# Performance work log

Hardware: AMD Instinct MI355X
Metric: run time of the kernel (lower is better)

## Reference

```python
import jax, jax.numpy as jnp
import numpy as np

L = 28          # layers
D = 1024        # hidden
HQ = 16         # query heads
HKV = 8         # kv heads
HD = 128        # head dim
DFF = 3072      # mlp intermediate
Q = 512         # prefill length (= end_step, past_kv_len = 0)
EPS = 1e-6


def setup_inputs() -> dict:
    key = jax.random.key(0)
    ks = jax.random.split(key, 12)
    s = 0.02
    hidden_states = jax.random.normal(ks[0], (1, Q, D), jnp.float32)
    # RoPE tables (concatenated-halves layout, base 1e6 as in Qwen3)
    pos = jnp.arange(Q, dtype=jnp.float32)
    inv_freq = 1.0 / (1e6 ** (jnp.arange(0, HD, 2, dtype=jnp.float32) / HD))
    freqs = pos[:, None] * inv_freq[None, :]              # [Q, HD/2]
    emb = jnp.concatenate([freqs, freqs], axis=-1)        # [Q, HD]
    position_cos = jnp.cos(emb)[None]                     # [1, Q, HD]
    position_sin = jnp.sin(emb)[None]
    # causal mask: 0 where key_pos <= query_pos else -1e9 ; [1,1,Q,Q]
    i = jnp.arange(Q)
    attention_mask = jnp.where(i[None, :] <= i[:, None], 0.0, -1e9).astype(jnp.float32)[None, None]
    # stacked per-layer weights (torch Linear y = x @ W^T stored here as [in,out])
    Wq = jax.random.normal(ks[1], (L, D, HQ * HD), jnp.float32) * s
    Wk = jax.random.normal(ks[2], (L, D, HKV * HD), jnp.float32) * s
    Wv = jax.random.normal(ks[3], (L, D, HKV * HD), jnp.float32) * s
    Wo = jax.random.normal(ks[4], (L, HQ * HD, D), jnp.float32) * s
    Wg = jax.random.normal(ks[5], (L, D, DFF), jnp.float32) * s
    Wu = jax.random.normal(ks[6], (L, D, DFF), jnp.float32) * s
    Wd = jax.random.normal(ks[7], (L, DFF, D), jnp.float32) * s
    ln1 = jnp.ones((L, D), jnp.float32)
    ln2 = jnp.ones((L, D), jnp.float32)
    qn = jnp.ones((L, HD), jnp.float32)
    kn = jnp.ones((L, HD), jnp.float32)
    return {"hidden_states": hidden_states, "position_cos": position_cos,
            "position_sin": position_sin, "attention_mask": attention_mask,
            "Wq": Wq, "Wk": Wk, "Wv": Wv, "Wo": Wo, "Wg": Wg, "Wu": Wu, "Wd": Wd,
            "ln1": ln1, "ln2": ln2, "qn": qn, "kn": kn}


def rmsnorm(x, w):
    return x * jax.lax.rsqrt(jnp.mean(x * x, axis=-1, keepdims=True) + EPS) * w


def rotate_half(x):
    x1, x2 = jnp.split(x, 2, axis=-1)
    return jnp.concatenate([-x2, x1], axis=-1)


def reference(hidden_states, position_cos, position_sin, attention_mask,
              Wq, Wk, Wv, Wo, Wg, Wu, Wd, ln1, ln2, qn, kn):
    q_len = hidden_states.shape[1]
    scale = 1.0 / np.sqrt(HD)
    cos = position_cos[:, None]   # [1,1,Q,HD] broadcast over heads
    sin = position_sin[:, None]

    def layer(h, p):
        wq, wk, wv, wo, wg, wu, wd, l1, l2, qw, kw = p
        x = rmsnorm(h, l1)
        q = (x @ wq).reshape(1, q_len, HQ, HD).transpose(0, 2, 1, 3)   # [1,HQ,Q,HD]
        k = (x @ wk).reshape(1, q_len, HKV, HD).transpose(0, 2, 1, 3)  # [1,HKV,Q,HD]
        v = (x @ wv).reshape(1, q_len, HKV, HD).transpose(0, 2, 1, 3)
        q = rmsnorm(q, qw)
        k = rmsnorm(k, kw)
        q = q * cos + rotate_half(q) * sin
        k = k * cos + rotate_half(k) * sin
        # fp16 KV-cache round trip (faithful to k.half() store / .float() load)
        k = k.astype(jnp.float16).astype(jnp.float32)
        v = v.astype(jnp.float16).astype(jnp.float32)
        # GQA: repeat kv heads
        k = jnp.repeat(k, HQ // HKV, axis=1)
        v = jnp.repeat(v, HQ // HKV, axis=1)
        scores = jnp.einsum('bhqd,bhkd->bhqk', q, k) * scale + attention_mask
        probs = jax.nn.softmax(scores, axis=-1)
        attn = jnp.einsum('bhqk,bhkd->bhqd', probs, v)
        attn = attn.transpose(0, 2, 1, 3).reshape(1, q_len, HQ * HD)
        h = h + attn @ wo
        y = rmsnorm(h, l2)
        h = h + (jax.nn.silu(y @ wg) * (y @ wu)) @ wd
        return h, None

    params = (Wq, Wk, Wv, Wo, Wg, Wu, Wd, ln1, ln2, qn, kn)
    out, _ = jax.lax.scan(layer, hidden_states, params)
    return out
```

## Files before the change

### kernel.cpp

```cpp
#include <hip/hip_runtime.h>
#include <stdint.h>


typedef __bf16 bf16_t;
typedef _Float16 f16_t;
typedef __bf16 bf16x8 __attribute__((ext_vector_type(8)));
typedef __bf16 bf16x4 __attribute__((ext_vector_type(4)));
typedef _Float16 f16x8 __attribute__((ext_vector_type(8)));
typedef _Float16 f16x4 __attribute__((ext_vector_type(4)));
typedef float f32x4 __attribute__((ext_vector_type(4)));

#define SEQ 512
#define NHQ 16
#define NHKV 8
#define HD 128

#define IMG_QKV 0ull
#define IMG_WO  8388608ull
#define IMG_GU  12582912ull
#define IMG_WD  25165824ull
#define IMG_LAYER_BYTES 31457280ull

typedef const __attribute__((address_space(1))) uint32_t as1_u32;
typedef __attribute__((address_space(3))) uint32_t as3_u32;

__device__ __forceinline__ void gload16(const void* g, void* l) {
    __builtin_amdgcn_global_load_lds((as1_u32*)g, (as3_u32*)l, 16, 0, 0);
}

__device__ __forceinline__ size_t aoff(int row, int col, int ldak) {
    return (((size_t)((row >> 6) * ldak + (col >> 6))) << 13) +
           ((size_t)(row & 63) << 7) +
           (size_t)((((col & 63) << 1)) ^ ((row & 7) << 4));
}

__global__ __launch_bounds__(256) void k_copy(const float* __restrict__ src,
                                              float* __restrict__ dst)
{
    size_t i = ((size_t)blockIdx.x * 256 + threadIdx.x) * 4;
    *(float4*)(dst + i) = *(const float4*)(src + i);
}

__device__ __forceinline__ void conv_tile(
    int b, int lay,
    const float* __restrict__ Wq, const float* __restrict__ Wk,
    const float* __restrict__ Wv, const float* __restrict__ Wo,
    const float* __restrict__ Wg, const float* __restrict__ Wu,
    const float* __restrict__ Wd, char* __restrict__ ib, void* smemv)
{
    const float* wq = Wq + (size_t)lay * 1024 * 2048;
    const float* wk = Wk + (size_t)lay * 1024 * 1024;
    const float* wv = Wv + (size_t)lay * 1024 * 1024;
    const float* wo = Wo + (size_t)lay * 2048 * 1024;
    const float* wg = Wg + (size_t)lay * 1024 * 3072;
    const float* wu = Wu + (size_t)lay * 1024 * 3072;
    const float* wd = Wd + (size_t)lay * 3072 * 1024;

    const float* src = nullptr;
    int ldbw = 0, n, kt, guMode = 0;
    size_t dstoff;
    if (b < 1024) {
        n = b >> 4; kt = b & 15;
        int C0 = n * 64;
        if (C0 < 2048)      { src = wq + C0;          ldbw = 2048; }
        else if (C0 < 3072) { src = wk + (C0 - 2048); ldbw = 1024; }
        else                { src = wv + (C0 - 3072); ldbw = 1024; }
        src += (size_t)(kt * 64) * ldbw;
        dstoff = IMG_QKV + (size_t)b * 8192;
    } else if (b < 1536) {
        int b2 = b - 1024; n = b2 >> 5; kt = b2 & 31;
        src = wo + (size_t)(kt * 64) * 1024 + n * 64; ldbw = 1024;
        dstoff = IMG_WO + (size_t)b2 * 8192;
    } else if (b < 3072) {
        int b3 = b - 1536; n = b3 >> 4; kt = b3 & 15;
        guMode = 1; ldbw = 3072;
        dstoff = IMG_GU + (size_t)b3 * 8192;
    } else {
        int b4 = b - 3072; n = b4 / 48; kt = b4 % 48;
        src = wd + (size_t)(kt * 64) * 1024 + n * 64; ldbw = 1024;
        dstoff = IMG_WD + (size_t)b4 * 8192;
    }

    float (*T)[68] = (float (*)[68])smemv;
    int tid = threadIdx.x;
    if (!guMode) {
#pragma unroll
        for (int it = 0; it < 4; ++it) {
            int idx = it * 256 + tid;
            int kk = idx >> 4, seg = idx & 15;
            *(float4*)&T[kk][seg * 4] = *(const float4*)(src + (size_t)kk * ldbw + seg * 4);
        }
    } else {
        const float* wg_ = wg + (size_t)(kt * 64) * 3072;
        const float* wu_ = wu + (size_t)(kt * 64) * 3072;
#pragma unroll
        for (int it = 0; it < 4; ++it) {
            int idx = it * 256 + tid;
            int kk = idx >> 4, seg = idx & 15;
            int nl = seg * 4;
            int colc = n * 32 + ((nl >> 5) & 1) * 16 + (nl & 15);
            const float* s2 = (((nl >> 4) & 1) ? wu_ : wg_) + (size_t)kk * 3072 + colc;
            *(float4*)&T[kk][nl] = *(const float4*)s2;
        }
    }
    __syncthreads();
    char* dst = ib + dstoff;
#pragma unroll
    for (int it = 0; it < 2; ++it) {
        int kg = tid & 7;
        int nrow = it * 32 + (tid >> 3);
        bf16x8 o;
#pragma unroll
        for (int j = 0; j < 8; ++j) o[j] = (bf16_t)T[kg * 8 + j][nrow];
        *(bf16x8*)(dst + nrow * 128 + ((kg * 16) ^ ((nrow & 7) << 4))) = o;
    }
}

__global__ __launch_bounds__(256) void k_conv(
    int lay,
    const float* __restrict__ Wq, const float* __restrict__ Wk,
    const float* __restrict__ Wv, const float* __restrict__ Wo,
    const float* __restrict__ Wg, const float* __restrict__ Wu,
    const float* __restrict__ Wd, char* __restrict__ img)
{
    __shared__ __align__(16) char smem[17408];
    conv_tile(blockIdx.x, lay, Wq, Wk, Wv, Wo, Wg, Wu, Wd, img, smem);
}

__global__ __launch_bounds__(256) void k_rms(
    float* __restrict__ h, const bf16_t* __restrict__ parts, int nparts,
    const float* __restrict__ w, char* __restrict__ ximg)
{
    int t = blockIdx.x, tid = threadIdx.x;
    size_t base = (size_t)t * 1024 + tid * 4;
    float4 v = *(const float4*)(h + base);
    for (int p = 0; p < nparts; ++p) {
        bf16x4 a = *(const bf16x4*)(parts + (size_t)p * 524288 + base);
        v.x += (float)a[0]; v.y += (float)a[1]; v.z += (float)a[2]; v.w += (float)a[3];
    }
    if (nparts) *(float4*)(h + base) = v;
    float ss = v.x * v.x + v.y * v.y + v.z * v.z + v.w * v.w;
#pragma unroll
    for (int m = 1; m < 64; m <<= 1) ss += __shfl_xor(ss, m);
    __shared__ float red[4];
    if ((tid & 63) == 0) red[tid >> 6] = ss;
    __syncthreads();
    float tot = (red[0] + red[1]) + (red[2] + red[3]);
    float sc = rsqrtf(tot * (1.0f / 1024.0f) + 1e-6f);
    float4 wv4 = *(const float4*)(w + tid * 4);
    bf16x4 o;
    o[0] = (bf16_t)(v.x * sc * wv4.x);
    o[1] = (bf16_t)(v.y * sc * wv4.y);
    o[2] = (bf16_t)(v.z * sc * wv4.z);
    o[3] = (bf16_t)(v.w * sc * wv4.w);
    *(bf16x4*)(ximg + aoff(t, tid * 4, 16)) = o;
}

__global__ __launch_bounds__(256) void k_finalize(
    const float* __restrict__ h, const bf16_t* __restrict__ parts,
    float* __restrict__ out)
{
    size_t base = ((size_t)blockIdx.x * 256 + threadIdx.x) * 4;
    float4 v = *(const float4*)(h + base);
#pragma unroll
    for (int p = 0; p < 4; ++p) {
        bf16x4 a = *(const bf16x4*)(parts + (size_t)p * 524288 + base);
        v.x += (float)a[0]; v.y += (float)a[1]; v.z += (float)a[2]; v.w += (float)a[3];
    }
    *(float4*)(out + base) = v;
}

template <int NBN, int SPLITK, int MODE, int LDAK>
__device__ __forceinline__ void gemm_core(
    const char* __restrict__ Aimg, const char* __restrict__ Bimg,
    void* __restrict__ outp, char* smem, int f)
{
    const int steps = LDAK / SPLITK;
    int bm = f / (NBN * SPLITK);
    int r = f % (NBN * SPLITK);
    int s = r / NBN;
    int bn = r % NBN;
    int k0d = s * steps;

    int tid = threadIdx.x;
    int wv = tid >> 6, l = tid & 63, lg = l >> 4, lr = l & 15;
    int wr = wv >> 1, wc = wv & 1;

    f32x4 acc[2][4];
#pragma unroll
    for (int i = 0; i < 2; ++i)
#pragma unroll
        for (int j = 0; j < 4; ++j) { f32x4 z = {0.f, 0.f, 0.f, 0.f}; acc[i][j] = z; }

    auto stage = [&](int buf, int kt) {
        const char* ab = Aimg + ((size_t)(bm * LDAK + k0d + kt)) * 8192;
        const char* b0 = Bimg + ((size_t)((2 * bn) * LDAK + k0d + kt)) * 8192;
        const char* b1 = Bimg + ((size_t)((2 * bn + 1) * LDAK + k0d + kt)) * 8192;
        char* al = smem + buf * 24576;
        char* bl = al + 8192;
#pragma unroll
        for (int u = 0; u < 2; ++u) {
            int off = (wv * 2 + u) * 1024;
            gload16(ab + off + l * 16, al + off);
        }
#pragma unroll
        for (int u = 0; u < 4; ++u) {
            int off = (wv * 4 + u) * 1024;
            const char* src = (off < 8192) ? (b0 + off) : (b1 + off - 8192);
            gload16(src + l * 16, bl + off);
        }
    };
    auto compute = [&](int buf) {
        const char* as = smem + buf * 24576;
        const char* bs = as + 8192 + wc * 8192;
#pragma unroll
        for (int c = 0; c < 2; ++c) {
            int co = (c * 64 + lg * 16) ^ ((lr & 7) << 4);
            bf16x8 af[2], bf[4];
#pragma unroll
            for (int i = 0; i < 2; ++i)
                af[i] = *(const bf16x8*)(as + (wr * 32 + i * 16 + lr) * 128 + co);
#pragma unroll
            for (int j = 0; j < 4; ++j)
                bf[j] = *(const bf16x8*)(bs + (j * 16 + lr) * 128 + co);
#pragma unroll
            for (int i = 0; i < 2; ++i)
#pragma unroll
                for (int j = 0; j < 4; ++j)
                    acc[i][j] = __builtin_amdgcn_mfma_f32_16x16x32_bf16(
                        af[i], bf[j], acc[i][j], 0, 0, 0);
        }
    };

    stage(0, 0);
    __syncthreads();
    int buf = 0;
    for (int kt = 0; kt < steps; ++kt) {
        if (kt + 1 < steps) stage(buf ^ 1, kt + 1);
        compute(buf);
        __syncthreads();
        buf ^= 1;
    }

    if (MODE == 0) {
        bf16_t* P = (bf16_t*)outp + (size_t)s * 524288;
#pragma unroll
        for (int i = 0; i < 2; ++i)
#pragma unroll
            for (int j = 0; j < 4; ++j)
#pragma unroll
                for (int ii = 0; ii < 4; ++ii) {
                    int row = bm * 64 + wr * 32 + i * 16 + lg * 4 + ii;
                    int col = bn * 128 + wc * 64 + j * 16 + lr;
                    P[(size_t)row * 1024 + col] = (bf16_t)acc[i][j][ii];
                }
    } else if (MODE == 2) {
        f16_t* Q = (f16_t*)outp;
#pragma unroll
        for (int i = 0; i < 2; ++i)
#pragma unroll
            for (int j = 0; j < 4; ++j)
#pragma unroll
                for (int ii = 0; ii < 4; ++ii) {
                    int row = bm * 64 + wr * 32 + i * 16 + lg * 4 + ii;
                    int col = bn * 128 + wc * 64 + j * 16 + lr;
                    Q[(size_t)row * 4096 + col] = (f16_t)acc[i][j][ii];
                }
    } else {
        char* M = (char*)outp;
#pragma unroll
        for (int i = 0; i < 2; ++i)
#pragma unroll
            for (int jp = 0; jp < 2; ++jp)
#pragma unroll
                for (int ii = 0; ii < 4; ++ii) {
                    int row = bm * 64 + wr * 32 + i * 16 + lg * 4 + ii;
                    int col = (bn * 2 + wc) * 32 + jp * 16 + lr;
                    float gv = acc[i][2 * jp][ii];
                    float uv = acc[i][2 * jp + 1][ii];
                    float val = gv / (1.f + __expf(-gv)) * uv;
                    *(bf16_t*)(M + aoff(row, col, 48)) = (bf16_t)val;
                }
    }
}

__global__ __launch_bounds__(256) void g_qkv(const char* A, const char* B, f16_t* out)
{
    __shared__ __align__(128) char smem[49152];
    gemm_core<32, 1, 2, 16>(A, B, out, smem, blockIdx.x);
}
__global__ __launch_bounds__(256) void g_wo(const char* A, const char* B, bf16_t* parts)
{
    __shared__ __align__(128) char smem[49152];
    gemm_core<8, 4, 0, 32>(A, B, parts, smem, blockIdx.x);
}
__global__ __launch_bounds__(256) void g_gu(const char* A, const char* B, char* mimg)
{
    __shared__ __align__(128) char smem[49152];
    gemm_core<48, 1, 1, 16>(A, B, mimg, smem, blockIdx.x);
}
__global__ __launch_bounds__(256) void k_wdc(
    const char* A, const char* B, bf16_t* parts,
    const float* Wq, const float* Wk, const float* Wv, const float* Wo,
    const float* Wg, const float* Wu, const float* Wd,
    int lnext, char* imgnext)
{
    __shared__ __align__(128) char smem[49152];
    int b = blockIdx.x;
    if (b < 256) gemm_core<8, 4, 0, 48>(A, B, parts, smem, b);
    else conv_tile(b - 256, lnext, Wq, Wk, Wv, Wo, Wg, Wu, Wd, imgnext, smem);
}

__global__ __launch_bounds__(256) void k_qv(
    const f16_t* __restrict__ qkvh,
    const float* __restrict__ qw, const float* __restrict__ kw,
    const float* __restrict__ cosb, const float* __restrict__ sinb,
    f16_t* __restrict__ qf, f16_t* __restrict__ kf, f16_t* __restrict__ vT)
{
    int b = blockIdx.x;
    int tid = threadIdx.x;
    if (b < 3072) {
        int idx = b * 4 + (tid >> 6);
        int slot = idx % 24;
        int t = idx / 24;
        int d = tid & 63;
        bool isq = slot < 16;
        int col = isq ? slot * HD + d : 2048 + (slot - 16) * HD + d;
        const f16_t* row = qkvh + (size_t)t * 4096;
        float x1 = (float)row[col];
        float x2 = (float)row[col + 64];
        float ss = x1 * x1 + x2 * x2;
#pragma unroll
        for (int m = 1; m < 64; m <<= 1) ss += __shfl_xor(ss, m);
        float sc = rsqrtf(ss * (1.0f / 128.0f) + 1e-6f);
        float w1 = isq ? qw[d] : kw[d];
        float w2 = isq ? qw[d + 64] : kw[d + 64];
        float xn1 = x1 * sc * w1, xn2 = x2 * sc * w2;
        float o1 = xn1 * cosb[t * HD + d] - xn2 * sinb[t * HD + d];
        float o2 = xn2 * cosb[t * HD + d + 64] + xn1 * sinb[t * HD + d + 64];
        if (isq) {
            f16_t* o = qf + ((size_t)slot * SEQ + t) * HD;
            o[d] = (f16_t)o1; o[d + 64] = (f16_t)o2;
        } else {
            f16_t* o = kf + ((size_t)(slot - 16) * SEQ + t) * HD;
            o[d] = (f16_t)o1; o[d + 64] = (f16_t)o2;
        }
    } else {
        __shared__ f16_t tileS[128][136];
        int vb = b - 3072;
        int kvh = vb >> 2, tb = vb & 3;
#pragma unroll
        for (int it = 0; it < 8; ++it) {
            int r = it * 16 + (tid >> 4);
            int cs = tid & 15;
            f16x8 v = *(const f16x8*)(qkvh + (size_t)(tb * 128 + r) * 4096 + 3072 + kvh * HD + cs * 8);
            *(f16x8*)&tileS[r][cs * 8] = v;
        }
        __syncthreads();
#pragma unroll
        for (int it = 0; it < 8; ++it) {
            int dr = it * 16 + (tid >> 4);
            int seg = tid & 15;
            f16x8 o;
#pragma unroll
            for (int j = 0; j < 8; ++j) o[j] = tileS[seg * 8 + j][dr];
            *(f16x8*)(vT + ((size_t)kvh * HD + dr) * SEQ + tb * 128 + seg * 8) = o;
        }
    }
}

__global__ __launch_bounds__(128) void k_attn(
    const f16_t* __restrict__ qf, const f16_t* __restrict__ kf,
    const f16_t* __restrict__ vT, char* __restrict__ attimg)
{
    int h = blockIdx.x >> 4, qb = blockIdx.x & 15;
    int kvh = h >> 1;
    __shared__ f16_t Kt[64][136];
    __shared__ f16_t Vt[128][72];
    __shared__ f16_t Pl[2][16][72];
    int tid = threadIdx.x;
    int wv = tid >> 6, l = tid & 63, lg = l >> 4, lr = l & 15;
    int q0 = qb * 32;
    int qrow = q0 + wv * 16;

    f16x8 aq[4];
    const f16_t* qp = qf + ((size_t)h * SEQ + qrow + lr) * HD;
#pragma unroll
    for (int c = 0; c < 4; ++c) aq[c] = *(const f16x8*)(qp + c * 32 + lg * 8);

    f32x4 accv[8];
#pragma unroll
    for (int df = 0; df < 8; ++df) { f32x4 z = {0.f, 0.f, 0.f, 0.f}; accv[df] = z; }
    float mrun[4], lrun[4];
#pragma unroll
    for (int ii = 0; ii < 4; ++ii) { mrun[ii] = -3e38f; lrun[ii] = 0.f; }

    int ktiles = (q0 + 32 + 63) >> 6;
    for (int kt = 0; kt < ktiles; ++kt) {
        int kt0 = kt * 64;
        __syncthreads();
#pragma unroll
        for (int it = 0; it < 8; ++it) {
            int idx = it * 128 + tid;
            int r = idx >> 4, seg = idx & 15;
            *(int4*)&Kt[r][seg * 8] =
                *(const int4*)(kf + ((size_t)kvh * SEQ + kt0 + r) * HD + seg * 8);
        }
#pragma unroll
        for (int it = 0; it < 8; ++it) {
            int idx = it * 128 + tid;
            int r = idx >> 3, seg = idx & 7;
            *(int4*)&Vt[r][seg * 8] =
                *(const int4*)(vT + ((size_t)kvh * HD + r) * SEQ + kt0 + seg * 8);
        }
        __syncthreads();

        f32x4 s[4];
#pragma unroll
        for (int nf = 0; nf < 4; ++nf) {
            f32x4 a = {0.f, 0.f, 0.f, 0.f};
#pragma unroll
            for (int c = 0; c < 4; ++c) {
                f16x8 bk = *(const f16x8*)&Kt[nf * 16 + lr][c * 32 + lg * 8];
                a = __builtin_amdgcn_mfma_f32_16x16x32_f16(aq[c], bk, a, 0, 0, 0);
            }
            s[nf] = a;
        }
        const float scale = 0.08838834764831845f;
        float tmax[4] = {-3e38f, -3e38f, -3e38f, -3e38f};
#pragma unroll
        for (int nf = 0; nf < 4; ++nf) {
            int ktg = kt0 + nf * 16 + lr;
#pragma unroll
            for (int ii = 0; ii < 4; ++ii) {
                int qg = qrow + lg * 4 + ii;
                float vv = s[nf][ii] * scale;
                vv = (ktg <= qg) ? vv : -1e30f;
                s[nf][ii] = vv;
                tmax[ii] = fmaxf(tmax[ii], vv);
            }
        }
#pragma unroll
        for (int m = 1; m < 16; m <<= 1)
#pragma unroll
            for (int ii = 0; ii < 4; ++ii)
                tmax[ii] = fmaxf(tmax[ii], __shfl_xor(tmax[ii], m));
        float corr[4];
#pragma unroll
        for (int ii = 0; ii < 4; ++ii) {
            float mnew = fmaxf(mrun[ii], tmax[ii]);
            corr[ii] = __expf(mrun[ii] - mnew);
            mrun[ii] = mnew;
        }
        float tsum[4] = {0.f, 0.f, 0.f, 0.f};
#pragma unroll
        for (int nf = 0; nf < 4; ++nf)
#pragma unroll
            for (int ii = 0; ii < 4; ++ii) {
                float pp = __expf(s[nf][ii] - mrun[ii]);
                s[nf][ii] = pp;
                tsum[ii] += pp;
            }
#pragma unroll
        for (int m = 1; m < 16; m <<= 1)
#pragma unroll
            for (int ii = 0; ii < 4; ++ii) tsum[ii] += __shfl_xor(tsum[ii], m);
#pragma unroll
        for (int ii = 0; ii < 4; ++ii) lrun[ii] = lrun[ii] * corr[ii] + tsum[ii];
#pragma unroll
        for (int df = 0; df < 8; ++df)
#pragma unroll
            for (int ii = 0; ii < 4; ++ii) accv[df][ii] *= corr[ii];
#pragma unroll
        for (int nf = 0; nf < 4; ++nf)
#pragma unroll
            for (int ii = 0; ii < 4; ++ii)
                Pl[wv][lg * 4 + ii][nf * 16 + lr] = (f16_t)s[nf][ii];
        __syncthreads();
#pragma unroll
        for (int c = 0; c < 2; ++c) {
            f16x8 ap = *(const f16x8*)&Pl[wv][lr][c * 32 + lg * 8];
#pragma unroll
            for (int df = 0; df < 8; ++df) {
                f16x8 bv = *(const f16x8*)&Vt[df * 16 + lr][c * 32 + lg * 8];
                accv[df] = __builtin_amdgcn_mfma_f32_16x16x32_f16(ap, bv, accv[df], 0, 0, 0);
            }
        }
    }
#pragma unroll
    for (int df = 0; df < 8; ++df)
#pragma unroll
        for (int ii = 0; ii < 4; ++ii) {
            int qg = qrow + lg * 4 + ii;
            int col = h * HD + df * 16 + lr;
            *(bf16_t*)(attimg + aoff(qg, col, 32)) =
                (bf16_t)(accv[df][ii] / lrun[ii]);
        }
}

extern "C" void kernel_launch(void* const* d_in, const int* in_sizes, int n_in,
                              void* d_out, int out_size, void* d_ws, size_t ws_size,
                              hipStream_t stream)
{
    const float* hin  = (const float*)d_in[0];
    const float* cosb = (const float*)d_in[1];
    const float* sinb = (const float*)d_in[2];
    const float* Wq = (const float*)d_in[4];
    const float* Wk = (const float*)d_in[5];
    const float* Wv = (const float*)d_in[6];
    const float* Wo = (const float*)d_in[7];
    const float* Wg = (const float*)d_in[8];
    const float* Wu = (const float*)d_in[9];
    const float* Wd = (const float*)d_in[10];
    const float* Ln1 = (const float*)d_in[11];
    const float* Ln2 = (const float*)d_in[12];
    const float* Qn = (const float*)d_in[13];
    const float* Kn = (const float*)d_in[14];

    char* p = (char*)d_ws;
    auto alloc = [&](size_t bytes) { char* r = p; p += bytes; return r; };
    float*  h     = (float*)alloc(2097152);
    bf16_t* parts = (bf16_t*)alloc(4194304);
    char*   ximg  = alloc(1048576);
    char*   yimg  = alloc(1048576);
    char*   attimg= alloc(2097152);
    char*   mimg  = alloc(3145728);
    f16_t*  qkvh  = (f16_t*)alloc(4194304);
    f16_t*  qf    = (f16_t*)alloc(2097152);
    f16_t*  kf    = (f16_t*)alloc(1048576);
    f16_t*  vT    = (f16_t*)alloc(1048576);
    char*   imgA  = alloc(IMG_LAYER_BYTES);
    size_t fixed = (size_t)(imgA + IMG_LAYER_BYTES - (char*)d_ws);
    bool pp = ws_size >= fixed + IMG_LAYER_BYTES;
    char* imgB = pp ? alloc(IMG_LAYER_BYTES) : imgA;

    k_copy<<<512, 256, 0, stream>>>(hin, h);
    k_conv<<<3840, 256, 0, stream>>>(0, Wq, Wk, Wv, Wo, Wg, Wu, Wd, imgA);

    for (int l = 0; l < 28; ++l) {
        char* img  = (l & 1) ? imgB : imgA;
        char* imgn = (l & 1) ? imgA : imgB;

        k_rms<<<512, 256, 0, stream>>>(h, parts, l == 0 ? 0 : 4,
                                       Ln1 + (size_t)l * 1024, ximg);
        g_qkv<<<256, 256, 0, stream>>>(ximg, img + IMG_QKV, qkvh);
        k_qv<<<3104, 256, 0, stream>>>(qkvh, Qn + (size_t)l * 128,
                                       Kn + (size_t)l * 128, cosb, sinb,
                                       qf, kf, vT);
        k_attn<<<256, 128, 0, stream>>>(qf, kf, vT, attimg);
        g_wo<<<256, 256, 0, stream>>>(attimg, img + IMG_WO, parts);
        k_rms<<<512, 256, 0, stream>>>(h, parts, 4, Ln2 + (size_t)l * 1024, yimg);
        g_gu<<<384, 256, 0, stream>>>(yimg, img + IMG_GU, mimg);

        bool fuse = pp && (l < 27);
        k_wdc<<<fuse ? 4096 : 256, 256, 0, stream>>>(
            mimg, img + IMG_WD, parts, Wq, Wk, Wv, Wo, Wg, Wu, Wd,
            l + 1, imgn);
        if (!pp && l < 27)
            k_conv<<<3840, 256, 0, stream>>>(l + 1, Wq, Wk, Wv, Wo, Wg, Wu, Wd, imgA);
    }
    k_finalize<<<512, 256, 0, stream>>>(h, parts, (float*)d_out);
}
```

Before: 2.568 ms.

## Fuse QK-norm, RoPE and V transpose into QKV GEMM epilogue; refine pipeline waits

The QKV GEMM epilogue now stages the fp32 tile in shared memory and applies per-head RMSNorm, RoPE and the V transpose itself, writing qf/kf/vT directly. This removes the separate k_qv launch and the fp16 qkvh round trip through global memory. The GEMM main loop also swaps full __syncthreads for explicit vmcnt waits plus s_barrier, and raises wave priority around the MFMA block so loads can overlap compute. The cost is a heavier, more serialized epilogue in 256 blocks, and the hand-written waitcnt has to match the number of loads issued per stage.

```diff
diff --git a/kernel.cpp b/kernel.cpp
--- a/kernel.cpp
+++ b/kernel.cpp
@@ -7,7 +7,6 @@
 typedef __bf16 bf16x8 __attribute__((ext_vector_type(8)));
 typedef __bf16 bf16x4 __attribute__((ext_vector_type(4)));
 typedef _Float16 f16x8 __attribute__((ext_vector_type(8)));
-typedef _Float16 f16x4 __attribute__((ext_vector_type(4)));
 typedef float f32x4 __attribute__((ext_vector_type(4)));
 
 #define SEQ 512
@@ -27,6 +26,9 @@
 __device__ __forceinline__ void gload16(const void* g, void* l) {
     __builtin_amdgcn_global_load_lds((as1_u32*)g, (as3_u32*)l, 16, 0, 0);
 }
+
+#define WAITV6 asm volatile("s_waitcnt vmcnt(6)" ::: "memory")
+#define WAITV0 asm volatile("s_waitcnt vmcnt(0)" ::: "memory")
 
 __device__ __forceinline__ size_t aoff(int row, int col, int ldak) {
     return (((size_t)((row >> 6) * ldak + (col >> 6))) << 13) +
@@ -170,10 +172,10 @@
     *(float4*)(out + base) = v;
 }
 
-template <int NBN, int SPLITK, int MODE, int LDAK>
-__device__ __forceinline__ void gemm_core(
+template <int NBN, int SPLITK, int LDAK>
+__device__ __forceinline__ void gemm_loop(
     const char* __restrict__ Aimg, const char* __restrict__ Bimg,
-    void* __restrict__ outp, char* smem, int f)
+    char* smem, int f, f32x4 (&acc)[2][4], int& bmO, int& bnO, int& sO)
 {
     const int steps = LDAK / SPLITK;
     int bm = f / (NBN * SPLITK);
@@ -181,12 +183,12 @@
     int s = r / NBN;
     int bn = r % NBN;
     int k0d = s * steps;
+    bmO = bm; bnO = bn; sO = s;
 
     int tid = threadIdx.x;
     int wv = tid >> 6, l = tid & 63, lg = l >> 4, lr = l & 15;
     int wr = wv >> 1, wc = wv & 1;
 
-    f32x4 acc[2][4];
 #pragma unroll
     for (int i = 0; i < 2; ++i)
 #pragma unroll
@@ -213,6 +215,7 @@
     auto compute = [&](int buf) {
         const char* as = smem + buf * 24576;
         const char* bs = as + 8192 + wc * 8192;
+        __builtin_amdgcn_s_setprio(1);
 #pragma unroll
         for (int c = 0; c < 2; ++c) {
             int co = (c * 64 + lg * 16) ^ ((lr & 7) << 4);
@@ -230,75 +233,163 @@
                     acc[i][j] = __builtin_amdgcn_mfma_f32_16x16x32_bf16(
                         af[i], bf[j], acc[i][j], 0, 0, 0);
         }
+        __builtin_amdgcn_s_setprio(0);
     };
 
     stage(0, 0);
-    __syncthreads();
     int buf = 0;
     for (int kt = 0; kt < steps; ++kt) {
-        if (kt + 1 < steps) stage(buf ^ 1, kt + 1);
+        if (kt + 1 < steps) { stage(buf ^ 1, kt + 1); WAITV6; }
+        else                { WAITV0; }
+        __builtin_amdgcn_sched_barrier(0);
+        __builtin_amdgcn_s_barrier();
+        __builtin_amdgcn_sched_barrier(0);
         compute(buf);
-        __syncthreads();
+        __builtin_amdgcn_s_barrier();
         buf ^= 1;
     }
-
-    if (MODE == 0) {
-        bf16_t* P = (bf16_t*)outp + (size_t)s * 524288;
-#pragma unroll
-        for (int i = 0; i < 2; ++i)
-#pragma unroll
-            for (int j = 0; j < 4; ++j)
-#pragma unroll
-                for (int ii = 0; ii < 4; ++ii) {
-                    int row = bm * 64 + wr * 32 + i * 16 + lg * 4 + ii;
-                    int col = bn * 128 + wc * 64 + j * 16 + lr;
-                    P[(size_t)row * 1024 + col] = (bf16_t)acc[i][j][ii];
-                }
-    } else if (MODE == 2) {
-        f16_t* Q = (f16_t*)outp;
-#pragma unroll
-        for (int i = 0; i < 2; ++i)
-#pragma unroll
-            for (int j = 0; j < 4; ++j)
-#pragma unroll
-                for (int ii = 0; ii < 4; ++ii) {
-                    int row = bm * 64 + wr * 32 + i * 16 + lg * 4 + ii;
-                    int col = bn * 128 + wc * 64 + j * 16 + lr;
-                    Q[(size_t)row * 4096 + col] = (f16_t)acc[i][j][ii];
-                }
+}
+
+__global__ __launch_bounds__(256) void g_qkvf(
+    const char* __restrict__ Aimg, const char* __restrict__ Bimg,
+    const float* __restrict__ cosb, const float* __restrict__ sinb,
+    const float* __restrict__ qw, const float* __restrict__ kw,
+    f16_t* __restrict__ qf, f16_t* __restrict__ kf, f16_t* __restrict__ vT)
+{
+    __shared__ __align__(128) char smem[49152];
+    f32x4 acc[2][4];
+    int bm, bn, s;
+    gemm_loop<32, 1, 16>(Aimg, Bimg, smem, blockIdx.x, acc, bm, bn, s);
+
+    int tid = threadIdx.x;
+    int wv = tid >> 6, l = tid & 63, lg = l >> 4, lr = l & 15;
+    int wr = wv >> 1, wc = wv & 1;
+    float (*X)[132] = (float (*)[132])smem;
+#pragma unroll
+    for (int i = 0; i < 2; ++i)
+#pragma unroll
+        for (int j = 0; j < 4; ++j)
+#pragma unroll
+            for (int ii = 0; ii < 4; ++ii)
+                X[wr * 32 + i * 16 + lg * 4 + ii][wc * 64 + j * 16 + lr] = acc[i][j][ii];
+    __syncthreads();
+
+    int t0 = bm * 64;
+    if (bn < 24) {
+        bool isq = bn < 16;
+        int slot = isq ? bn : bn - 16;
+        const float* wn = isq ? qw : kw;
+        int r = tid >> 2, part = tid & 3;
+        float ss = 0.f;
+#pragma unroll
+        for (int c = 0; c < 32; ++c) { float v = X[r][part * 32 + c]; ss += v * v; }
+        ss += __shfl_xor(ss, 1);
+        ss += __shfl_xor(ss, 2);
+        float sc = rsqrtf(ss * (1.0f / 128.0f) + 1e-6f);
+        int t = t0 + r;
+        int d0 = part * 16;
+        float o1v[16], o2v[16];
+#pragma unroll
+        for (int c = 0; c < 16; ++c) {
+            int d = d0 + c;
+            float xv1 = X[r][d] * sc * wn[d];
+            float xv2 = X[r][d + 64] * sc * wn[d + 64];
+            o1v[c] = xv1 * cosb[t * HD + d] - xv2 * sinb[t * HD + d];
+            o2v[c] = xv2 * cosb[t * HD + d + 64] + xv1 * sinb[t * HD + d + 64];
+        }
+        f16x8 w0, w1, w2, w3;
+#pragma unroll
+        for (int c = 0; c < 8; ++c) {
+            w0[c] = (f16_t)o1v[c];     w1[c] = (f16_t)o1v[8 + c];
+            w2[c] = (f16_t)o2v[c];     w3[c] = (f16_t)o2v[8 + c];
+        }
+        f16_t* o = (isq ? qf : kf) + ((size_t)slot * SEQ + t) * HD;
+        *(f16x8*)(o + d0) = w0;
+        *(f16x8*)(o + d0 + 8) = w1;
+        *(f16x8*)(o + d0 + 64) = w2;
+        *(f16x8*)(o + d0 + 72) = w3;
     } else {
-        char* M = (char*)outp;
-#pragma unroll
-        for (int i = 0; i < 2; ++i)
-#pragma unroll
-            for (int jp = 0; jp < 2; ++jp)
-#pragma unroll
-                for (int ii = 0; ii < 4; ++ii) {
-                    int row = bm * 64 + wr * 32 + i * 16 + lg * 4 + ii;
-                    int col = (bn * 2 + wc) * 32 + jp * 16 + lr;
-                    float gv = acc[i][2 * jp][ii];
-                    float uv = acc[i][2 * jp + 1][ii];
-                    float val = gv / (1.f + __expf(-gv)) * uv;
-                    *(bf16_t*)(M + aoff(row, col, 48)) = (bf16_t)val;
-                }
-    }
-}
-
-__global__ __launch_bounds__(256) void g_qkv(const char* A, const char* B, f16_t* out)
+        int kvh = bn - 24;
+#pragma unroll
+        for (int it = 0; it < 4; ++it) {
+            int task = it * 256 + tid;
+            int d = task >> 3, seg = task & 7;
+            f16x8 o;
+#pragma unroll
+            for (int j = 0; j < 8; ++j) o[j] = (f16_t)X[seg * 8 + j][d];
+            *(f16x8*)(vT + ((size_t)kvh * HD + d) * SEQ + t0 + seg * 8) = o;
+        }
+    }
+}
+
+__global__ __launch_bounds__(256) void g_wo(const char* A, const char* B, bf16_t* parts)
 {
     __shared__ __align__(128) char smem[49152];
-    gemm_core<32, 1, 2, 16>(A, B, out, smem, blockIdx.x);
-}
-__global__ __launch_bounds__(256) void g_wo(const char* A, const char* B, bf16_t* parts)
+    f32x4 acc[2][4];
+    int bm, bn, s;
+    gemm_loop<8, 4, 32>(A, B, smem, blockIdx.x, acc, bm, bn, s);
+    int tid = threadIdx.x;
+    int wv = tid >> 6, l = tid & 63, lg = l >> 4, lr = l & 15;
+    int wr = wv >> 1, wc = wv & 1;
+    bf16_t* P = parts + (size_t)s * 524288;
+#pragma unroll
+    for (int i = 0; i < 2; ++i)
+#pragma unroll
+        for (int j = 0; j < 4; ++j)
+#pragma unroll
+            for (int ii = 0; ii < 4; ++ii) {
+                int row = bm * 64 + wr * 32 + i * 16 + lg * 4 + ii;
+                int col = bn * 128 + wc * 64 + j * 16 + lr;
+                P[(size_t)row * 1024 + col] = (bf16_t)acc[i][j][ii];
+            }
+}
+
+__device__ __forceinline__ void wd_gemm(const char* A, const char* B,
+                                        bf16_t* parts, char* smem, int f)
+{
+    f32x4 acc[2][4];
+    int bm, bn, s;
+    gemm_loop<8, 4, 48>(A, B, smem, f, acc, bm, bn, s);
+    int tid = threadIdx.x;
+    int wv = tid >> 6, l = tid & 63, lg = l >> 4, lr = l & 15;
+    int wr = wv >> 1, wc = wv & 1;
+    bf16_t* P = parts + (size_t)s * 524288;
+#pragma unroll
+    for (int i = 0; i < 2; ++i)
+#pragma unroll
+        for (int j = 0; j < 4; ++j)
+#pragma unroll
+            for (int ii = 0; ii < 4; ++ii) {
+                int row = bm * 64 + wr * 32 + i * 16 + lg * 4 + ii;
+                int col = bn * 128 + wc * 64 + j * 16 + lr;
+                P[(size_t)row * 1024 + col] = (bf16_t)acc[i][j][ii];
+            }
+}
+
+__global__ __launch_bounds__(256) void g_gu(const char* A, const char* B, char* mimg)
 {
     __shared__ __align__(128) char smem[49152];
-    gemm_core<8, 4, 0, 32>(A, B, parts, smem, blockIdx.x);
-}
-__global__ __launch_bounds__(256) void g_gu(const char* A, const char* B, char* mimg)
-{
-    __shared__ __align__(128) char smem[49152];
-    gemm_core<48, 1, 1, 16>(A, B, mimg, smem, blockIdx.x);
-}
+    f32x4 acc[2][4];
+    int bm, bn, s;
+    gemm_loop<48, 1, 16>(A, B, smem, blockIdx.x, acc, bm, bn, s);
+    int tid = threadIdx.x;
+    int wv = tid >> 6, l = tid & 63, lg = l >> 4, lr = l & 15;
+    int wr = wv >> 1, wc = wv & 1;
+#pragma unroll
+    for (int i = 0; i < 2; ++i)
+#pragma unroll
+        for (int jp = 0; jp < 2; ++jp)
+#pragma unroll
+            for (int ii = 0; ii < 4; ++ii) {
+                int row = bm * 64 + wr * 32 + i * 16 + lg * 4 + ii;
+                int col = (bn * 2 + wc) * 32 + jp * 16 + lr;
+                float gv = acc[i][2 * jp][ii];
+                float uv = acc[i][2 * jp + 1][ii];
+                float val = gv / (1.f + __expf(-gv)) * uv;
+                *(bf16_t*)(mimg + aoff(row, col, 48)) = (bf16_t)val;
+            }
+}
+
 __global__ __launch_bounds__(256) void k_wdc(
     const char* A, const char* B, bf16_t* parts,
     const float* Wq, const float* Wk, const float* Wv, const float* Wo,
@@ -307,66 +398,8 @@
 {
     __shared__ __align__(128) char smem[49152];
     int b = blockIdx.x;
-    if (b < 256) gemm_core<8, 4, 0, 48>(A, B, parts, smem, b);
+    if (b < 256) wd_gemm(A, B, parts, smem, b);
     else conv_tile(b - 256, lnext, Wq, Wk, Wv, Wo, Wg, Wu, Wd, imgnext, smem);
-}
-
-__global__ __launch_bounds__(256) void k_qv(
-    const f16_t* __restrict__ qkvh,
-    const float* __restrict__ qw, const float* __restrict__ kw,
-    const float* __restrict__ cosb, const float* __restrict__ sinb,
-    f16_t* __restrict__ qf, f16_t* __restrict__ kf, f16_t* __restrict__ vT)
-{
-    int b = blockIdx.x;
-    int tid = threadIdx.x;
-    if (b < 3072) {
-        int idx = b * 4 + (tid >> 6);
-        int slot = idx % 24;
-        int t = idx / 24;
-        int d = tid & 63;
-        bool isq = slot < 16;
-        int col = isq ? slot * HD + d : 2048 + (slot - 16) * HD + d;
-        const f16_t* row = qkvh + (size_t)t * 4096;
-        float x1 = (float)row[col];
-        float x2 = (float)row[col + 64];
-        float ss = x1 * x1 + x2 * x2;
-#pragma unroll
-        for (int m = 1; m < 64; m <<= 1) ss += __shfl_xor(ss, m);
-        float sc = rsqrtf(ss * (1.0f / 128.0f) + 1e-6f);
-        float w1 = isq ? qw[d] : kw[d];
-        float w2 = isq ? qw[d + 64] : kw[d + 64];
-        float xn1 = x1 * sc * w1, xn2 = x2 * sc * w2;
-        float o1 = xn1 * cosb[t * HD + d] - xn2 * sinb[t * HD + d];
-        float o2 = xn2 * cosb[t * HD + d + 64] + xn1 * sinb[t * HD + d + 64];
-        if (isq) {
-            f16_t* o = qf + ((size_t)slot * SEQ + t) * HD;
-            o[d] = (f16_t)o1; o[d + 64] = (f16_t)o2;
-        } else {
-            f16_t* o = kf + ((size_t)(slot - 16) * SEQ + t) * HD;
-            o[d] = (f16_t)o1; o[d + 64] = (f16_t)o2;
-        }
-    } else {
-        __shared__ f16_t tileS[128][136];
-        int vb = b - 3072;
-        int kvh = vb >> 2, tb = vb & 3;
-#pragma unroll
-        for (int it = 0; it < 8; ++it) {
-            int r = it * 16 + (tid >> 4);
-            int cs = tid & 15;
-            f16x8 v = *(const f16x8*)(qkvh + (size_t)(tb * 128 + r) * 4096 + 3072 + kvh * HD + cs * 8);
-            *(f16x8*)&tileS[r][cs * 8] = v;
-        }
-        __syncthreads();
-#pragma unroll
-        for (int it = 0; it < 8; ++it) {
-            int dr = it * 16 + (tid >> 4);
-            int seg = tid & 15;
-            f16x8 o;
-#pragma unroll
-            for (int j = 0; j < 8; ++j) o[j] = tileS[seg * 8 + j][dr];
-            *(f16x8*)(vT + ((size_t)kvh * HD + dr) * SEQ + tb * 128 + seg * 8) = o;
-        }
-    }
 }
 
 __global__ __launch_bounds__(128) void k_attn(
@@ -525,7 +558,6 @@
     char*   yimg  = alloc(1048576);
     char*   attimg= alloc(2097152);
     char*   mimg  = alloc(3145728);
-    f16_t*  qkvh  = (f16_t*)alloc(4194304);
     f16_t*  qf    = (f16_t*)alloc(2097152);
     f16_t*  kf    = (f16_t*)alloc(1048576);
     f16_t*  vT    = (f16_t*)alloc(1048576);
@@ -543,10 +575,9 @@
 
         k_rms<<<512, 256, 0, stream>>>(h, parts, l == 0 ? 0 : 4,
                                        Ln1 + (size_t)l * 1024, ximg);
-        g_qkv<<<256, 256, 0, stream>>>(ximg, img + IMG_QKV, qkvh);
-        k_qv<<<3104, 256, 0, stream>>>(qkvh, Qn + (size_t)l * 128,
-                                       Kn + (size_t)l * 128, cosb, sinb,
-                                       qf, kf, vT);
+        g_qkvf<<<256, 256, 0, stream>>>(ximg, img + IMG_QKV, cosb, sinb,
+                                        Qn + (size_t)l * 128, Kn + (size_t)l * 128,
+                                        qf, kf, vT);
         k_attn<<<256, 128, 0, stream>>>(qf, kf, vT, attimg);
         g_wo<<<256, 256, 0, stream>>>(attimg, img + IMG_WO, parts);
         k_rms<<<512, 256, 0, stream>>>(h, parts, 4, Ln2 + (size_t)l * 1024, yimg);
```

Result: faster. 2.354 ms (-8.3%).
